# Performance work log

Hardware: AMD Instinct MI355X
Metric: run time of the kernel (lower is better)

Reference implementation:

```python
import jax, jax.numpy as jnp
import numpy as np

BS, OBJ, RNN, HID = 128, 512, 1024, 512

def setup_inputs() -> dict:
    key = jax.random.key(0)
    k = jax.random.split(key, 7)
    h = jax.random.normal(k[0], (BS, RNN), dtype=jnp.float32)
    att_feats = jax.random.normal(k[1], (BS, OBJ, HID), dtype=jnp.float32)
    att_masks = jax.random.randint(k[2], (BS, OBJ), 0, 2, dtype=jnp.int32)
    # nn.Linear params (PyTorch stores weight as [out, in])
    W_h2att = jax.random.normal(k[3], (HID, RNN), dtype=jnp.float32) / np.sqrt(RNN)
    b_h2att = jax.random.normal(k[4], (HID,), dtype=jnp.float32) * 0.02
    w_alpha = jax.random.normal(k[5], (HID,), dtype=jnp.float32) / np.sqrt(HID)
    b_alpha = jax.random.normal(k[6], (), dtype=jnp.float32) * 0.02
    return {"h": h, "att_feats": att_feats, "att_masks": att_masks,
            "W_h2att": W_h2att, "b_h2att": b_h2att,
            "w_alpha": w_alpha, "b_alpha": b_alpha}

def reference(h, att_feats, att_masks, W_h2att, b_h2att, w_alpha, b_alpha):
    # h2att: [bs, rnn] -> [bs, hid]
    att_h = h @ W_h2att.T + b_h2att
    # broadcast over objects, tanh, rank-1 projection to scalar score
    dot = jnp.tanh(att_feats + att_h[:, None, :])          # [bs, obj, hid]
    scores = jnp.einsum('boh,h->bo', dot, w_alpha) + b_alpha  # [bs, obj]
    weight = jax.nn.softmax(scores, axis=1)
    m = att_masks.astype(weight.dtype)
    weight = weight * m
    weight = weight / jnp.sum(weight, axis=1, keepdims=True)
    return weight
```

## Files before the change

### kernel.cpp

```cpp
#include <hip/hip_runtime.h>
#include <math.h>

#define BS  128
#define OBJ 512
#define RNN 1024
#define HID 512

__device__ __forceinline__ float combine2(float x, float y, int w) {
    int lane = threadIdx.x & 63;
    float send  = (lane & w) ? x : y;
    float other = __shfl_xor(send, w, 64);
    float keep  = (lane & w) ? y : x;
    return keep + other;
}

__device__ __forceinline__ float dot4(float4 a, float4 b, float s) {
    s = fmaf(a.x, b.x, s);
    s = fmaf(a.y, b.y, s);
    s = fmaf(a.z, b.z, s);
    s = fmaf(a.w, b.w, s);
    return s;
}

__global__ __launch_bounds__(256) void k1_h2att(
    const float* __restrict__ h, const float* __restrict__ W,
    float* __restrict__ att_h)
{
    const int lane = threadIdx.x & 63;
    const int wv   = blockIdx.x * 4 + (threadIdx.x >> 6);
    const int b0   = (wv >> 6) * 2;
    const int j0   = (wv & 63) * 8;

    const float4* h4 = (const float4*)h;
    const float4* W4 = (const float4*)W;

    float4 ha[2][4];
#pragma unroll
    for (int bi = 0; bi < 2; ++bi)
#pragma unroll
        for (int i = 0; i < 4; ++i)
            ha[bi][i] = h4[(b0 + bi) * 256 + i * 64 + lane];

    float acc[16];
#pragma unroll
    for (int jj = 0; jj < 8; ++jj) {
        const int wbase = (j0 + jj) * 256;
        float4 w0 = W4[wbase + 0 * 64 + lane];
        float4 w1 = W4[wbase + 1 * 64 + lane];
        float4 w2 = W4[wbase + 2 * 64 + lane];
        float4 w3 = W4[wbase + 3 * 64 + lane];
#pragma unroll
        for (int bi = 0; bi < 2; ++bi) {
            float s = 0.f;
            s = dot4(ha[bi][0], w0, s);
            s = dot4(ha[bi][1], w1, s);
            s = dot4(ha[bi][2], w2, s);
            s = dot4(ha[bi][3], w3, s);
            acc[jj * 2 + bi] = s;
        }
    }

    float t8[8];
#pragma unroll
    for (int i = 0; i < 8; ++i) t8[i] = combine2(acc[2 * i], acc[2 * i + 1], 1);
    float t4v[4];
#pragma unroll
    for (int i = 0; i < 4; ++i) t4v[i] = combine2(t8[2 * i], t8[2 * i + 1], 2);
    float t2v[2];
#pragma unroll
    for (int i = 0; i < 2; ++i) t2v[i] = combine2(t4v[2 * i], t4v[2 * i + 1], 4);
    float t1 = combine2(t2v[0], t2v[1], 8);
    t1 += __shfl_xor(t1, 16, 64);
    t1 += __shfl_xor(t1, 32, 64);

    if (lane < 16) {
        int bi = lane & 1;
        int jj = lane >> 1;
        att_h[(b0 + bi) * HID + j0 + jj] = t1;
    }
}

__global__ __launch_bounds__(256, 4) void k2_scores(
    const float* __restrict__ att_feats, const float* __restrict__ att_h,
    const float* __restrict__ b_h2att, const float* __restrict__ w_alpha,
    float* __restrict__ scores)
{
    const int lane = threadIdx.x & 63;
    const int wv   = blockIdx.x * 4 + (threadIdx.x >> 6);
    const int b    = wv >> 6;
    const int o0   = (wv & 63) * 8;

    const float4* f4 = (const float4*)att_feats + (size_t)(b * OBJ + o0) * 128;

    float4 x[16];
#pragma unroll
    for (int oo = 0; oo < 8; ++oo) {
        x[2 * oo]     = f4[oo * 128 + lane];
        x[2 * oo + 1] = f4[oo * 128 + 64 + lane];
    }

    const float C = 2.8853900817779268f;
    const float4* ah4 = (const float4*)(att_h + b * HID);
    const float4* bb4 = (const float4*)b_h2att;
    const float4* wa4 = (const float4*)w_alpha;

    float4 a0 = ah4[lane],  a1 = ah4[64 + lane];
    float4 c0 = bb4[lane],  c1 = bb4[64 + lane];
    float4 wa0 = wa4[lane], wa1 = wa4[64 + lane];

    float4 hs0, hs1;
    hs0.x = (a0.x + c0.x) * C; hs0.y = (a0.y + c0.y) * C;
    hs0.z = (a0.z + c0.z) * C; hs0.w = (a0.w + c0.w) * C;
    hs1.x = (a1.x + c1.x) * C; hs1.y = (a1.y + c1.y) * C;
    hs1.z = (a1.z + c1.z) * C; hs1.w = (a1.w + c1.w) * C;

    float wsum = wa0.x + wa0.y + wa0.z + wa0.w + wa1.x + wa1.y + wa1.z + wa1.w;

    float acc[8];
#pragma unroll
    for (int oo = 0; oo < 8; ++oo) {
        const float4 x0 = x[2 * oo];
        const float4 x1 = x[2 * oo + 1];
        float s = 0.f;
        s = fmaf(wa0.x, __builtin_amdgcn_rcpf(exp2f(fmaf(x0.x, C, hs0.x)) + 1.0f), s);
        s = fmaf(wa0.y, __builtin_amdgcn_rcpf(exp2f(fmaf(x0.y, C, hs0.y)) + 1.0f), s);
        s = fmaf(wa0.z, __builtin_amdgcn_rcpf(exp2f(fmaf(x0.z, C, hs0.z)) + 1.0f), s);
        s = fmaf(wa0.w, __builtin_amdgcn_rcpf(exp2f(fmaf(x0.w, C, hs0.w)) + 1.0f), s);
        s = fmaf(wa1.x, __builtin_amdgcn_rcpf(exp2f(fmaf(x1.x, C, hs1.x)) + 1.0f), s);
        s = fmaf(wa1.y, __builtin_amdgcn_rcpf(exp2f(fmaf(x1.y, C, hs1.y)) + 1.0f), s);
        s = fmaf(wa1.z, __builtin_amdgcn_rcpf(exp2f(fmaf(x1.z, C, hs1.z)) + 1.0f), s);
        s = fmaf(wa1.w, __builtin_amdgcn_rcpf(exp2f(fmaf(x1.w, C, hs1.w)) + 1.0f), s);
        acc[oo] = s;
    }

    float t4v[4];
#pragma unroll
    for (int i = 0; i < 4; ++i) t4v[i] = combine2(acc[2 * i], acc[2 * i + 1], 1);
    float t2v[2];
#pragma unroll
    for (int i = 0; i < 2; ++i) t2v[i] = combine2(t4v[2 * i], t4v[2 * i + 1], 2);
    float t1 = combine2(t2v[0], t2v[1], 4);
    t1 += __shfl_xor(t1, 8, 64);
    t1 += __shfl_xor(t1, 16, 64);
    t1 += __shfl_xor(t1, 32, 64);

    float tw = wsum;
#pragma unroll
    for (int w = 1; w <= 32; w <<= 1) tw += __shfl_xor(tw, w, 64);

    if (lane < 8) scores[b * OBJ + o0 + lane] = tw - 2.0f * t1;
}

__global__ __launch_bounds__(256) void k3_softmax(
    float* __restrict__ scores_out, const int* __restrict__ masks)
{
    __shared__ float red[4];
    const int b    = blockIdx.x;
    const int t    = threadIdx.x;
    const int lane = t & 63;
    const int wv   = t >> 6;

    float s0 = scores_out[b * OBJ + t];
    float s1 = scores_out[b * OBJ + t + 256];
    float m0 = (float)masks[b * OBJ + t];
    float m1 = (float)masks[b * OBJ + t + 256];

    float mx = fmaxf(s0, s1);
#pragma unroll
    for (int w = 1; w <= 32; w <<= 1) mx = fmaxf(mx, __shfl_xor(mx, w, 64));
    if (lane == 0) red[wv] = mx;
    __syncthreads();
    mx = fmaxf(fmaxf(red[0], red[1]), fmaxf(red[2], red[3]));
    __syncthreads();

    float e0 = __expf(s0 - mx) * m0;
    float e1 = __expf(s1 - mx) * m1;
    float sm = e0 + e1;
#pragma unroll
    for (int w = 1; w <= 32; w <<= 1) sm += __shfl_xor(sm, w, 64);
    if (lane == 0) red[wv] = sm;
    __syncthreads();
    sm = (red[0] + red[1]) + (red[2] + red[3]);

    float inv = 1.0f / sm;
    scores_out[b * OBJ + t]       = e0 * inv;
    scores_out[b * OBJ + t + 256] = e1 * inv;
}

extern "C" void kernel_launch(void* const* d_in, const int* in_sizes, int n_in,
                              void* d_out, int out_size, void* d_ws, size_t ws_size,
                              hipStream_t stream)
{
    const float* h         = (const float*)d_in[0];
    const float* att_feats = (const float*)d_in[1];
    const int*   att_masks = (const int*)d_in[2];
    const float* W_h2att   = (const float*)d_in[3];
    const float* b_h2att   = (const float*)d_in[4];
    const float* w_alpha   = (const float*)d_in[5];

    float* att_h  = (float*)d_ws;
    float* scores = (float*)d_out;

    k1_h2att  <<<dim3(1024), dim3(256), 0, stream>>>(h, W_h2att, att_h);
    k2_scores <<<dim3(2048), dim3(256), 0, stream>>>(att_feats, att_h, b_h2att,
                                                     w_alpha, scores);
    k3_softmax<<<dim3(BS),   dim3(256), 0, stream>>>(scores, att_masks);
}
```

Baseline: 216.9 us.

## Fuse h2att, score and masked softmax into one per-batch kernel

Replaces the three kernels with a single kernel that uses one 1024-thread block per batch row. Each block computes its row of att_h into LDS, then the tanh scores. It applies the softmax without subtracting the max, stores the masked exponentials in LDS, accumulates their sum with an LDS atomic, and normalises. This removes two launches and the global round-trips for att_h and scores. The trade-offs: only 128 blocks run on a 256-CU device, every block rereads the full W matrix, and dropping the max subtraction relies on scores staying small enough that exp does not overflow.

```diff
diff --git a/kernel.cpp b/kernel.cpp
--- a/kernel.cpp
+++ b/kernel.cpp
@@ -22,169 +22,137 @@
     return s;
 }
 
-__global__ __launch_bounds__(256) void k1_h2att(
-    const float* __restrict__ h, const float* __restrict__ W,
-    float* __restrict__ att_h)
+__global__ __launch_bounds__(1024, 4) void fused1(
+    const float* __restrict__ h, const float* __restrict__ att_feats,
+    const int* __restrict__ masks, const float* __restrict__ W,
+    const float* __restrict__ b_h2att, const float* __restrict__ w_alpha,
+    float* __restrict__ out)
 {
+    __shared__ float lds_hs[HID];
+    __shared__ float ebuf[OBJ];
+    __shared__ float lds_sum;
+
+    const int b    = blockIdx.x;
     const int lane = threadIdx.x & 63;
-    const int wv   = blockIdx.x * 4 + (threadIdx.x >> 6);
-    const int b0   = (wv >> 6) * 2;
-    const int j0   = (wv & 63) * 8;
+    const int wv   = threadIdx.x >> 6;
+    const float C  = 2.8853900817779268f;
 
-    const float4* h4 = (const float4*)h;
-    const float4* W4 = (const float4*)W;
+    if (threadIdx.x == 0) lds_sum = 0.0f;
 
-    float4 ha[2][4];
+    {
+        const float4* h4 = (const float4*)h;
+        const float4* W4 = (const float4*)W;
+
+        float4 ha[4];
 #pragma unroll
-    for (int bi = 0; bi < 2; ++bi)
+        for (int i = 0; i < 4; ++i) ha[i] = h4[b * 256 + i * 64 + lane];
+
 #pragma unroll
-        for (int i = 0; i < 4; ++i)
-            ha[bi][i] = h4[(b0 + bi) * 256 + i * 64 + lane];
-
-    float acc[16];
+        for (int g = 0; g < 4; ++g) {
+            const int j0 = wv * 32 + g * 8;
+            float acc[8];
 #pragma unroll
-    for (int jj = 0; jj < 8; ++jj) {
-        const int wbase = (j0 + jj) * 256;
-        float4 w0 = W4[wbase + 0 * 64 + lane];
-        float4 w1 = W4[wbase + 1 * 64 + lane];
-        float4 w2 = W4[wbase + 2 * 64 + lane];
-        float4 w3 = W4[wbase + 3 * 64 + lane];
+            for (int jj = 0; jj < 8; ++jj) {
+                const int wbase = (j0 + jj) * 256;
+                float4 w0 = W4[wbase + 0 * 64 + lane];
+                float4 w1 = W4[wbase + 1 * 64 + lane];
+                float4 w2 = W4[wbase + 2 * 64 + lane];
+                float4 w3 = W4[wbase + 3 * 64 + lane];
+                float s = 0.f;
+                s = dot4(ha[0], w0, s);
+                s = dot4(ha[1], w1, s);
+                s = dot4(ha[2], w2, s);
+                s = dot4(ha[3], w3, s);
+                acc[jj] = s;
+            }
+            float t4v[4];
 #pragma unroll
-        for (int bi = 0; bi < 2; ++bi) {
-            float s = 0.f;
-            s = dot4(ha[bi][0], w0, s);
-            s = dot4(ha[bi][1], w1, s);
-            s = dot4(ha[bi][2], w2, s);
-            s = dot4(ha[bi][3], w3, s);
-            acc[jj * 2 + bi] = s;
+            for (int i = 0; i < 4; ++i) t4v[i] = combine2(acc[2 * i], acc[2 * i + 1], 1);
+            float t2v[2];
+#pragma unroll
+            for (int i = 0; i < 2; ++i) t2v[i] = combine2(t4v[2 * i], t4v[2 * i + 1], 2);
+            float t1 = combine2(t2v[0], t2v[1], 4);
+            t1 += __shfl_xor(t1, 8, 64);
+            t1 += __shfl_xor(t1, 16, 64);
+            t1 += __shfl_xor(t1, 32, 64);
+            if (lane < 8) {
+                const int j = j0 + lane;
+                lds_hs[j] = (t1 + b_h2att[j]) * C;
+            }
         }
     }
-
-    float t8[8];
-#pragma unroll
-    for (int i = 0; i < 8; ++i) t8[i] = combine2(acc[2 * i], acc[2 * i + 1], 1);
-    float t4v[4];
-#pragma unroll
-    for (int i = 0; i < 4; ++i) t4v[i] = combine2(t8[2 * i], t8[2 * i + 1], 2);
-    float t2v[2];
-#pragma unroll
-    for (int i = 0; i < 2; ++i) t2v[i] = combine2(t4v[2 * i], t4v[2 * i + 1], 4);
-    float t1 = combine2(t2v[0], t2v[1], 8);
-    t1 += __shfl_xor(t1, 16, 64);
-    t1 += __shfl_xor(t1, 32, 64);
-
-    if (lane < 16) {
-        int bi = lane & 1;
-        int jj = lane >> 1;
-        att_h[(b0 + bi) * HID + j0 + jj] = t1;
-    }
-}
-
-__global__ __launch_bounds__(256, 4) void k2_scores(
-    const float* __restrict__ att_feats, const float* __restrict__ att_h,
-    const float* __restrict__ b_h2att, const float* __restrict__ w_alpha,
-    float* __restrict__ scores)
-{
-    const int lane = threadIdx.x & 63;
-    const int wv   = blockIdx.x * 4 + (threadIdx.x >> 6);
-    const int b    = wv >> 6;
-    const int o0   = (wv & 63) * 8;
-
-    const float4* f4 = (const float4*)att_feats + (size_t)(b * OBJ + o0) * 128;
-
-    float4 x[16];
-#pragma unroll
-    for (int oo = 0; oo < 8; ++oo) {
-        x[2 * oo]     = f4[oo * 128 + lane];
-        x[2 * oo + 1] = f4[oo * 128 + 64 + lane];
-    }
-
-    const float C = 2.8853900817779268f;
-    const float4* ah4 = (const float4*)(att_h + b * HID);
-    const float4* bb4 = (const float4*)b_h2att;
-    const float4* wa4 = (const float4*)w_alpha;
-
-    float4 a0 = ah4[lane],  a1 = ah4[64 + lane];
-    float4 c0 = bb4[lane],  c1 = bb4[64 + lane];
-    float4 wa0 = wa4[lane], wa1 = wa4[64 + lane];
-
-    float4 hs0, hs1;
-    hs0.x = (a0.x + c0.x) * C; hs0.y = (a0.y + c0.y) * C;
-    hs0.z = (a0.z + c0.z) * C; hs0.w = (a0.w + c0.w) * C;
-    hs1.x = (a1.x + c1.x) * C; hs1.y = (a1.y + c1.y) * C;
-    hs1.z = (a1.z + c1.z) * C; hs1.w = (a1.w + c1.w) * C;
-
-    float wsum = wa0.x + wa0.y + wa0.z + wa0.w + wa1.x + wa1.y + wa1.z + wa1.w;
-
-    float acc[8];
-#pragma unroll
-    for (int oo = 0; oo < 8; ++oo) {
-        const float4 x0 = x[2 * oo];
-        const float4 x1 = x[2 * oo + 1];
-        float s = 0.f;
-        s = fmaf(wa0.x, __builtin_amdgcn_rcpf(exp2f(fmaf(x0.x, C, hs0.x)) + 1.0f), s);
-        s = fmaf(wa0.y, __builtin_amdgcn_rcpf(exp2f(fmaf(x0.y, C, hs0.y)) + 1.0f), s);
-        s = fmaf(wa0.z, __builtin_amdgcn_rcpf(exp2f(fmaf(x0.z, C, hs0.z)) + 1.0f), s);
-        s = fmaf(wa0.w, __builtin_amdgcn_rcpf(exp2f(fmaf(x0.w, C, hs0.w)) + 1.0f), s);
-        s = fmaf(wa1.x, __builtin_amdgcn_rcpf(exp2f(fmaf(x1.x, C, hs1.x)) + 1.0f), s);
-        s = fmaf(wa1.y, __builtin_amdgcn_rcpf(exp2f(fmaf(x1.y, C, hs1.y)) + 1.0f), s);
-        s = fmaf(wa1.z, __builtin_amdgcn_rcpf(exp2f(fmaf(x1.z, C, hs1.z)) + 1.0f), s);
-        s = fmaf(wa1.w, __builtin_amdgcn_rcpf(exp2f(fmaf(x1.w, C, hs1.w)) + 1.0f), s);
-        acc[oo] = s;
-    }
-
-    float t4v[4];
-#pragma unroll
-    for (int i = 0; i < 4; ++i) t4v[i] = combine2(acc[2 * i], acc[2 * i + 1], 1);
-    float t2v[2];
-#pragma unroll
-    for (int i = 0; i < 2; ++i) t2v[i] = combine2(t4v[2 * i], t4v[2 * i + 1], 2);
-    float t1 = combine2(t2v[0], t2v[1], 4);
-    t1 += __shfl_xor(t1, 8, 64);
-    t1 += __shfl_xor(t1, 16, 64);
-    t1 += __shfl_xor(t1, 32, 64);
-
-    float tw = wsum;
-#pragma unroll
-    for (int w = 1; w <= 32; w <<= 1) tw += __shfl_xor(tw, w, 64);
-
-    if (lane < 8) scores[b * OBJ + o0 + lane] = tw - 2.0f * t1;
-}
-
-__global__ __launch_bounds__(256) void k3_softmax(
-    float* __restrict__ scores_out, const int* __restrict__ masks)
-{
-    __shared__ float red[4];
-    const int b    = blockIdx.x;
-    const int t    = threadIdx.x;
-    const int lane = t & 63;
-    const int wv   = t >> 6;
-
-    float s0 = scores_out[b * OBJ + t];
-    float s1 = scores_out[b * OBJ + t + 256];
-    float m0 = (float)masks[b * OBJ + t];
-    float m1 = (float)masks[b * OBJ + t + 256];
-
-    float mx = fmaxf(s0, s1);
-#pragma unroll
-    for (int w = 1; w <= 32; w <<= 1) mx = fmaxf(mx, __shfl_xor(mx, w, 64));
-    if (lane == 0) red[wv] = mx;
-    __syncthreads();
-    mx = fmaxf(fmaxf(red[0], red[1]), fmaxf(red[2], red[3]));
     __syncthreads();
 
-    float e0 = __expf(s0 - mx) * m0;
-    float e1 = __expf(s1 - mx) * m1;
-    float sm = e0 + e1;
+    {
+        const float4* wa4 = (const float4*)w_alpha;
+        float4 wa0 = wa4[lane], wa1 = wa4[64 + lane];
+        const float4* hsl = (const float4*)lds_hs;
+        float4 hs0 = hsl[lane], hs1 = hsl[64 + lane];
+
+        float tw = wa0.x + wa0.y + wa0.z + wa0.w + wa1.x + wa1.y + wa1.z + wa1.w;
 #pragma unroll
-    for (int w = 1; w <= 32; w <<= 1) sm += __shfl_xor(sm, w, 64);
-    if (lane == 0) red[wv] = sm;
+        for (int w = 1; w <= 32; w <<= 1) tw += __shfl_xor(tw, w, 64);
+
+#pragma unroll
+        for (int p = 0; p < 4; ++p) {
+            const int o0 = (wv * 4 + p) * 8;
+            const float4* f4 = (const float4*)att_feats
+                               + ((size_t)b * OBJ + o0) * 128;
+
+            float4 x[16];
+#pragma unroll
+            for (int oo = 0; oo < 8; ++oo) {
+                x[2 * oo]     = f4[oo * 128 + lane];
+                x[2 * oo + 1] = f4[oo * 128 + 64 + lane];
+            }
+
+            float acc[8];
+#pragma unroll
+            for (int oo = 0; oo < 8; ++oo) {
+                const float4 x0 = x[2 * oo];
+                const float4 x1 = x[2 * oo + 1];
+                float s = 0.f;
+                s = fmaf(wa0.x, __builtin_amdgcn_rcpf(exp2f(fmaf(x0.x, C, hs0.x)) + 1.0f), s);
+                s = fmaf(wa0.y, __builtin_amdgcn_rcpf(exp2f(fmaf(x0.y, C, hs0.y)) + 1.0f), s);
+                s = fmaf(wa0.z, __builtin_amdgcn_rcpf(exp2f(fmaf(x0.z, C, hs0.z)) + 1.0f), s);
+                s = fmaf(wa0.w, __builtin_amdgcn_rcpf(exp2f(fmaf(x0.w, C, hs0.w)) + 1.0f), s);
+                s = fmaf(wa1.x, __builtin_amdgcn_rcpf(exp2f(fmaf(x1.x, C, hs1.x)) + 1.0f), s);
+                s = fmaf(wa1.y, __builtin_amdgcn_rcpf(exp2f(fmaf(x1.y, C, hs1.y)) + 1.0f), s);
+                s = fmaf(wa1.z, __builtin_amdgcn_rcpf(exp2f(fmaf(x1.z, C, hs1.z)) + 1.0f), s);
+                s = fmaf(wa1.w, __builtin_amdgcn_rcpf(exp2f(fmaf(x1.w, C, hs1.w)) + 1.0f), s);
+                acc[oo] = s;
+            }
+
+            float t4v[4];
+#pragma unroll
+            for (int i = 0; i < 4; ++i) t4v[i] = combine2(acc[2 * i], acc[2 * i + 1], 1);
+            float t2v[2];
+#pragma unroll
+            for (int i = 0; i < 2; ++i) t2v[i] = combine2(t4v[2 * i], t4v[2 * i + 1], 2);
+            float t1 = combine2(t2v[0], t2v[1], 4);
+            t1 += __shfl_xor(t1, 8, 64);
+            t1 += __shfl_xor(t1, 16, 64);
+            t1 += __shfl_xor(t1, 32, 64);
+
+            float e = 0.0f;
+            if (lane < 8) {
+                float sc = tw - 2.0f * t1;
+                float m  = (float)masks[b * OBJ + o0 + lane];
+                e = __expf(sc) * m;
+                ebuf[o0 + lane] = e;
+            }
+            float es = e;
+            es += __shfl_xor(es, 1, 64);
+            es += __shfl_xor(es, 2, 64);
+            es += __shfl_xor(es, 4, 64);
+            if (lane == 0) atomicAdd(&lds_sum, es);
+        }
+    }
     __syncthreads();
-    sm = (red[0] + red[1]) + (red[2] + red[3]);
 
-    float inv = 1.0f / sm;
-    scores_out[b * OBJ + t]       = e0 * inv;
-    scores_out[b * OBJ + t + 256] = e1 * inv;
+    if (threadIdx.x < OBJ) {
+        out[b * OBJ + threadIdx.x] = ebuf[threadIdx.x] / lds_sum;
+    }
 }
 
 extern "C" void kernel_launch(void* const* d_in, const int* in_sizes, int n_in,
@@ -198,11 +166,8 @@
     const float* b_h2att   = (const float*)d_in[4];
     const float* w_alpha   = (const float*)d_in[5];
 
-    float* att_h  = (float*)d_ws;
-    float* scores = (float*)d_out;
+    float* out = (float*)d_out;
 
-    k1_h2att  <<<dim3(1024), dim3(256), 0, stream>>>(h, W_h2att, att_h);
-    k2_scores <<<dim3(2048), dim3(256), 0, stream>>>(att_feats, att_h, b_h2att,
-                                                     w_alpha, scores);
-    k3_softmax<<<dim3(BS),   dim3(256), 0, stream>>>(scores, att_masks);
+    fused1<<<dim3(BS), dim3(1024), 0, stream>>>(h, att_feats, att_masks,
+                                                W_h2att, b_h2att, w_alpha, out);
 }
```

Result: slower. 230.2 us (+6.1%).
